# Kernel optimization log

Measured on AMD Instinct MI355X. Metric: run time of the kernel, lower is better.

The kernel has to match this reference:

```python
import jax, jax.numpy as jnp
import numpy as np

C = 1024
H = 16
D = C // H

def setup_inputs() -> dict:
    key = jax.random.key(0)
    ks = jax.random.split(key, 12)
    s = 1.0 / np.sqrt(C)
    inp = {
        "Q": jax.random.normal(ks[0], (2, 1024, C), jnp.float32),
        "K_in": jax.random.normal(ks[1], (2, 4096, C), jnp.float32),
        "V_in": jax.random.normal(ks[2], (2, 4096, C), jnp.float32),
        "V_bias": jax.random.normal(ks[3], (2, 4096), jnp.float32),
        "Wq_w": jax.random.uniform(ks[4], (C, C), jnp.float32, -s, s),
        "Wq_b": jax.random.uniform(ks[5], (C,), jnp.float32, -s, s),
        "Wk_w": jax.random.uniform(ks[6], (C, C), jnp.float32, -s, s),
        "Wk_b": jax.random.uniform(ks[7], (C,), jnp.float32, -s, s),
        "Wv_w": jax.random.uniform(ks[8], (C, C), jnp.float32, -s, s),
        "Wv_b": jax.random.uniform(ks[9], (C,), jnp.float32, -s, s),
        "Wo_w": jax.random.uniform(ks[10], (C, C), jnp.float32, -s, s),
        "Wo_b": jax.random.uniform(ks[11], (C,), jnp.float32, -s, s),
    }
    return inp

def reference(Q, K_in, V_in, V_bias, Wq_w, Wq_b, Wk_w, Wk_b, Wv_w, Wv_b, Wo_w, Wo_b):
    B, Lq, _ = Q.shape
    Lk = K_in.shape[1]
    # linear projections (torch Linear: x @ W.T + b), split heads -> [B,H,L,D]
    q = (Q @ Wq_w.T + Wq_b).reshape(B, Lq, H, D).transpose(0, 2, 1, 3)
    k = (K_in @ Wk_w.T + Wk_b).reshape(B, Lk, H, D).transpose(0, 2, 1, 3)
    v = (V_in @ Wv_w.T + Wv_b).reshape(B, Lk, H, D).transpose(0, 2, 1, 3)
    scale = 1.0 / np.sqrt(D).astype(np.float32)
    logits = jnp.einsum("bhqd,bhkd->bhqk", q, k) * scale
    logits = logits + V_bias[:, None, None, :]  # per-key additive bias
    attn = jax.nn.softmax(logits, axis=-1)      # dropout p=0.0 (eval)
    out = jnp.einsum("bhqk,bhkd->bhqd", attn, v)
    out = out.transpose(0, 2, 1, 3).reshape(B, Lq, C)
    return out @ Wo_w.T + Wo_b
```

## Files before the change

### kernel.cpp

```cpp
#include <hip/hip_runtime.h>


typedef __attribute__((ext_vector_type(8))) __bf16 bf16x8;
typedef __attribute__((ext_vector_type(4))) float f32x4;
typedef __attribute__((ext_vector_type(16))) float f32x16;

#define LOG2E 1.44269504f
#define MFIX 24.0f

__device__ __forceinline__ unsigned short f2bf(float f) {
  union { float f; unsigned u; } v; v.f = f;
  unsigned r = v.u + 0x7fffu + ((v.u >> 16) & 1u);
  return (unsigned short)(r >> 16);
}
__device__ __forceinline__ unsigned short f2h(float x) {
  _Float16 h = (_Float16)x;
  return __builtin_bit_cast(unsigned short, h);
}
__device__ __forceinline__ float h2f(unsigned short u) {
  return (float)__builtin_bit_cast(_Float16, u);
}

__device__ __forceinline__ f32x4 mfma16(bf16x8 a, bf16x8 b, f32x4 c) {
  return __builtin_amdgcn_mfma_f32_16x16x32_bf16(a, b, c, 0, 0, 0);
}
__device__ __forceinline__ f32x16 mfma32(bf16x8 a, bf16x8 b, f32x16 c) {
  return __builtin_amdgcn_mfma_f32_32x32x16_bf16(a, b, c, 0, 0, 0);
}

__device__ __forceinline__ unsigned pk2(float lo, float hi) {
  unsigned short a = __builtin_bit_cast(unsigned short, (__bf16)lo);
  unsigned short b = __builtin_bit_cast(unsigned short, (__bf16)hi);
  return (unsigned)a | ((unsigned)b << 16);
}

template <typename T>
__device__ __forceinline__ void gload16(const T* g, T* l) {
  __builtin_amdgcn_global_load_lds(
      (const __attribute__((address_space(1))) void*)g,
      (__attribute__((address_space(3))) void*)l, 16, 0, 0);
}

struct CvtJob { const float* src; unsigned short* dst; int n4; };
struct CvtArgs { CvtJob j[6]; };

__global__ __launch_bounds__(256) void cvt_kernel(CvtArgs a) {
  const CvtJob jb = a.j[blockIdx.y];
  const float4* s = (const float4*)jb.src;
  unsigned short* d = jb.dst;
  const int stride = gridDim.x * blockDim.x;
  for (int i = blockIdx.x * blockDim.x + threadIdx.x; i < jb.n4; i += stride) {
    float4 f = s[i];
    ushort4 u;
    u.x = f2bf(f.x); u.y = f2bf(f.y); u.z = f2bf(f.z); u.w = f2bf(f.w);
    ((ushort4*)d)[i] = u;
  }
}

__global__ __launch_bounds__(256) void prep_kb(const float* __restrict__ Vb,
                                               unsigned* __restrict__ kb) {
  const int i = blockIdx.x * 256 + threadIdx.x;
  const float x = Vb[i] * LOG2E;
  const unsigned short h = f2bf(x);
  union { unsigned u; float f; } hf; hf.u = (unsigned)h << 16;
  const unsigned short lo = f2bf(x - hf.f);
  kb[i] = (unsigned)h | ((unsigned)lo << 16);
}

struct ProjSeg {
  const unsigned short* A; const unsigned short* W; const float* bias;
  void* out; int mode; int Llog2; float oscale;
};
struct ProjArgs { ProjSeg s[2]; int start1; };

__global__ __launch_bounds__(256, 2) void proj_gemm(ProjArgs pa) {
  constexpr int K = 1024;
  __shared__ unsigned short Alds[2][128][64];
  __shared__ unsigned short Blds[2][128][64];

  const int bid = blockIdx.x;
  const int si = (bid >= pa.start1) ? 1 : 0;
  const ProjSeg sg = pa.s[si];
  const int local = bid - (si ? pa.start1 : 0);
  const int xcd = local & 7, jj = local >> 3;
  const int m0 = ((jj >> 3) * 8 + xcd) * 128;
  const int n0 = (jj & 7) * 128;

  const int tid = threadIdx.x;
  const int wid = tid >> 6, l = tid & 63;
  const int wr = wid >> 1, wc = wid & 1;
  const int lg = l >> 4, lm = l & 15;

  const int srow = wid * 8 + (l >> 3);
  const int scol = ((l & 7) ^ (l >> 3)) * 8;
  const unsigned short* aS = sg.A + (long)(m0 + srow) * K + scol;
  const unsigned short* bS = sg.W + (long)(n0 + srow) * K + scol;

  f32x4 acc[4][4] = {};

  auto issue = [&](int kt, int buf) {
#pragma unroll
    for (int c = 0; c < 4; ++c) {
      gload16(aS + ((long)c * 32) * K + kt * 64,
              &Alds[buf][c * 32 + wid * 8][0]);
      gload16(bS + ((long)c * 32) * K + kt * 64,
              &Blds[buf][c * 32 + wid * 8][0]);
    }
  };

  issue(0, 0);
  issue(1, 1);

  for (int t = 0; t < 16; ++t) {
    if (t < 15) asm volatile("s_waitcnt vmcnt(8)" ::: "memory");
    else        asm volatile("s_waitcnt vmcnt(0)" ::: "memory");
    __builtin_amdgcn_sched_barrier(0);
    __builtin_amdgcn_s_barrier();
    const int buf = t & 1;

#pragma unroll
    for (int kc = 0; kc < 2; ++kc) {
      bf16x8 af[4], bf[4];
#pragma unroll
      for (int i = 0; i < 4; ++i) {
        const int so = ((kc * 4 + lg) ^ (lm & 7)) * 8;
        af[i] = *(const bf16x8*)&Alds[buf][wr * 64 + i * 16 + lm][so];
        bf[i] = *(const bf16x8*)&Blds[buf][wc * 64 + i * 16 + lm][so];
      }
      __builtin_amdgcn_s_setprio(1);
      if (sg.mode == 1) {
#pragma unroll
        for (int i = 0; i < 4; ++i)
#pragma unroll
          for (int j = 0; j < 4; ++j)
            acc[i][j] = mfma16(bf[i], af[j], acc[i][j]);
      } else {
#pragma unroll
        for (int i = 0; i < 4; ++i)
#pragma unroll
          for (int j = 0; j < 4; ++j)
            acc[i][j] = mfma16(af[i], bf[j], acc[i][j]);
      }
      __builtin_amdgcn_s_setprio(0);
    }

    __builtin_amdgcn_s_barrier();
    if (t + 2 < 16) issue(t + 2, buf);
  }

  const int rr = lg * 4;
  if (sg.mode == 0) {
    const int Lmask = (1 << sg.Llog2) - 1;
    unsigned short* out = (unsigned short*)sg.out;
#pragma unroll
    for (int j = 0; j < 4; ++j) {
      const int n = n0 + wc * 64 + j * 16 + lm;
      const float bv = sg.bias[n];
      const int h = n >> 6, d = n & 63;
#pragma unroll
      for (int i = 0; i < 4; ++i)
#pragma unroll
        for (int r = 0; r < 4; ++r) {
          const int m = m0 + wr * 64 + i * 16 + rr + r;
          const int b = m >> sg.Llog2, li = m & Lmask;
          const long o = (((long)(b * 16 + h) << sg.Llog2) + li) * 64 + d;
          out[o] = f2bf((acc[i][j][r] + bv) * sg.oscale);
        }
    }
  } else if (sg.mode == 1) {
    unsigned short* out = (unsigned short*)sg.out;
#pragma unroll
    for (int i = 0; i < 4; ++i)
#pragma unroll
      for (int r = 0; r < 4; ++r) {
        const int n = n0 + wc * 64 + i * 16 + rr + r;
        const float bv = sg.bias[n];
        const int h = n >> 6, d = n & 63;
#pragma unroll
        for (int j = 0; j < 4; ++j) {
          const int m = m0 + wr * 64 + j * 16 + lm;
          const int b = m >> 12, lk = m & 4095;
          const long o = ((long)((b * 16 + h) * 64 + d)) * 4096 + lk;
          out[o] = f2bf(acc[i][j][r] + bv);
        }
      }
  } else {
    float* out = (float*)sg.out;
#pragma unroll
    for (int j = 0; j < 4; ++j) {
      const int n = n0 + wc * 64 + j * 16 + lm;
      const float bv = sg.bias[n];
#pragma unroll
      for (int i = 0; i < 4; ++i)
#pragma unroll
        for (int r = 0; r < 4; ++r) {
          const int m = m0 + wr * 64 + i * 16 + rr + r;
          out[(long)m * 1024 + n] = acc[i][j][r] + bv;
        }
    }
  }
}

__global__ __launch_bounds__(256, 2) void attn64(
    const unsigned short* __restrict__ qh, const unsigned short* __restrict__ kh,
    const unsigned short* __restrict__ vT, const unsigned* __restrict__ kb,
    unsigned short* __restrict__ Oh, float* __restrict__ ml, int nt) {
  __shared__ unsigned short Klds[2][64][64];
  __shared__ unsigned short Vlds[2][64][64];

  const int tid = threadIdx.x;
  const int wid = tid >> 6, lane = tid & 63;
  const int lq = lane & 31, hi = lane >> 5;
  const int bh = blockIdx.x, qb = blockIdx.y, sp = blockIdx.z;
  const int b = bh >> 4;
  const int qA = qb * 256 + wid * 64 + lq;
  const int kt0 = sp * nt;

  bf16x8 qrA[4], qrB[4];
  {
    const unsigned short* qp = qh + ((long)bh * 1024 + qA) * 64 + hi * 8;
#pragma unroll
    for (int dc = 0; dc < 4; ++dc) {
      qrA[dc] = *(const bf16x8*)(qp + dc * 16);
      qrB[dc] = *(const bf16x8*)(qp + 32 * 64 + dc * 16);
    }
  }

  union uv { uint4 u; bf16x8 v; };
  uv bq; bq.u = make_uint4(hi ? 0u : 0x3F803F80u, 0u, 0u, 0u);

  auto swap23 = [](int r) { return (r & 0x33) | ((r & 4) << 1) | ((r & 8) >> 1); };
  const int r0 = wid * 16 + (lane >> 3), r1 = r0 + 8;
  const int s0 = ((lane & 7) ^ (r0 & 7)) * 8;
  const int s1 = ((lane & 7) ^ (r1 & 7)) * 8;
  const unsigned short* kg0 =
      kh + ((long)bh * 4096 + kt0 * 64 + swap23(r0)) * 64 + s0;
  const unsigned short* kg1 =
      kh + ((long)bh * 4096 + kt0 * 64 + swap23(r1)) * 64 + s1;
  const unsigned short* vg0 = vT + ((long)bh * 64 + r0) * 4096 + kt0 * 64 + s0;
  const unsigned short* vg1 = vT + ((long)bh * 64 + r1) * 4096 + kt0 * 64 + s1;
  const unsigned* kbp = kb + b * 4096 + kt0 * 64;
  const int kbkey = swap23(lq);

  unsigned kbw0[2], kbw1[2];
  auto issue = [&](int t, int buf) {
    gload16(kg0 + (long)t * 4096, &Klds[buf][wid * 16][0]);
    gload16(kg1 + (long)t * 4096, &Klds[buf][wid * 16 + 8][0]);
    gload16(vg0 + t * 64, &Vlds[buf][wid * 16][0]);
    gload16(vg1 + t * 64, &Vlds[buf][wid * 16 + 8][0]);
    kbw0[buf] = kbp[t * 64 + kbkey];
    kbw1[buf] = kbp[t * 64 + 32 + kbkey];
  };
  issue(0, 0);
  issue(1, 1);

  const int rsw = lq & 7;
  float lA = 0.f, lB = 0.f;
  f32x16 oaA0 = {}, oaA1 = {}, oaB0 = {}, oaB1 = {};
  uv puA[4], puB[4];

  auto softmax = [&](const f32x16& sx0, const f32x16& sx1, float& lreg,
                     uv* pu) {
    float p[32];
#pragma unroll
    for (int r = 0; r < 16; ++r) {
      p[r] = __builtin_amdgcn_exp2f(sx0[r] - MFIX);
      p[16 + r] = __builtin_amdgcn_exp2f(sx1[r] - MFIX);
    }
    float s16[16];
#pragma unroll
    for (int i = 0; i < 16; ++i) s16[i] = p[i] + p[i + 16];
#pragma unroll
    for (int s = 8; s > 0; s >>= 1)
#pragma unroll
      for (int i = 0; i < 8; ++i)
        if (i < s) s16[i] += s16[i + s];
    lreg += s16[0] + __shfl_xor(s16[0], 32);
#pragma unroll
    for (int kc = 0; kc < 4; ++kc)
      pu[kc].u = make_uint4(pk2(p[kc * 8 + 0], p[kc * 8 + 1]),
                            pk2(p[kc * 8 + 2], p[kc * 8 + 3]),
                            pk2(p[kc * 8 + 4], p[kc * 8 + 5]),
                            pk2(p[kc * 8 + 6], p[kc * 8 + 7]));
  };

  for (int t = 0; t < nt; ++t) {
    const int buf = t & 1;
    if (t < nt - 1) asm volatile("s_waitcnt vmcnt(6)" ::: "memory");
    else            asm volatile("s_waitcnt vmcnt(0)" ::: "memory");
    __builtin_amdgcn_sched_barrier(0);
    __builtin_amdgcn_s_barrier();

    uv ka0, ka1;
    ka0.u = make_uint4(hi ? 0u : kbw0[buf], 0u, 0u, 0u);
    ka1.u = make_uint4(hi ? 0u : kbw1[buf], 0u, 0u, 0u);

    bf16x8 kf0[4], kf1[4];
#pragma unroll
    for (int dc = 0; dc < 4; ++dc) {
      const int so = ((dc * 2 + hi) ^ rsw) * 8;
      kf0[dc] = *(const bf16x8*)&Klds[buf][lq][so];
      kf1[dc] = *(const bf16x8*)&Klds[buf][32 + lq][so];
    }

    f32x16 sa0 = {}, sa1 = {}, sb0 = {}, sb1 = {};
    __builtin_amdgcn_s_setprio(1);
#pragma unroll
    for (int dc = 0; dc < 4; ++dc) {
      sa0 = mfma32(kf0[dc], qrA[dc], sa0);
      sa1 = mfma32(kf1[dc], qrA[dc], sa1);
      sb0 = mfma32(kf0[dc], qrB[dc], sb0);
      sb1 = mfma32(kf1[dc], qrB[dc], sb1);
    }
    sa0 = mfma32(ka0.v, bq.v, sa0);
    sa1 = mfma32(ka1.v, bq.v, sa1);
    sb0 = mfma32(ka0.v, bq.v, sb0);
    sb1 = mfma32(ka1.v, bq.v, sb1);
    __builtin_amdgcn_s_setprio(0);

    softmax(sa0, sa1, lA, puA);

    bf16x8 vf0[4], vf1[4];
#pragma unroll
    for (int kc = 0; kc < 4; ++kc) {
      const int so = ((kc * 2 + hi) ^ rsw) * 8;
      vf0[kc] = *(const bf16x8*)&Vlds[buf][lq][so];
      vf1[kc] = *(const bf16x8*)&Vlds[buf][32 + lq][so];
    }

    __builtin_amdgcn_s_setprio(1);
#pragma unroll
    for (int kc = 0; kc < 4; ++kc) {
      oaA0 = mfma32(vf0[kc], puA[kc].v, oaA0);
      oaA1 = mfma32(vf1[kc], puA[kc].v, oaA1);
    }
    __builtin_amdgcn_s_setprio(0);

    softmax(sb0, sb1, lB, puB);

    __builtin_amdgcn_s_setprio(1);
#pragma unroll
    for (int kc = 0; kc < 4; ++kc) {
      oaB0 = mfma32(vf0[kc], puB[kc].v, oaB0);
      oaB1 = mfma32(vf1[kc], puB[kc].v, oaB1);
    }
    __builtin_amdgcn_s_setprio(0);

    __builtin_amdgcn_s_barrier();
    if (t + 2 < nt) issue(t + 2, buf);
  }

  const float invA = 1.0f / lA, invB = 1.0f / lB;
  unsigned short* obA = Oh + (((long)sp * 32 + bh) * 1024 + qA) * 64 + hi * 4;
  unsigned short* obB = obA + 32 * 64;
#pragma unroll
  for (int g = 0; g < 4; ++g) {
    ushort4 u;
    u.x = f2h(oaA0[g * 4 + 0] * invA); u.y = f2h(oaA0[g * 4 + 1] * invA);
    u.z = f2h(oaA0[g * 4 + 2] * invA); u.w = f2h(oaA0[g * 4 + 3] * invA);
    *(ushort4*)(obA + g * 8) = u;
    u.x = f2h(oaA1[g * 4 + 0] * invA); u.y = f2h(oaA1[g * 4 + 1] * invA);
    u.z = f2h(oaA1[g * 4 + 2] * invA); u.w = f2h(oaA1[g * 4 + 3] * invA);
    *(ushort4*)(obA + 32 + g * 8) = u;
    u.x = f2h(oaB0[g * 4 + 0] * invB); u.y = f2h(oaB0[g * 4 + 1] * invB);
    u.z = f2h(oaB0[g * 4 + 2] * invB); u.w = f2h(oaB0[g * 4 + 3] * invB);
    *(ushort4*)(obB + g * 8) = u;
    u.x = f2h(oaB1[g * 4 + 0] * invB); u.y = f2h(oaB1[g * 4 + 1] * invB);
    u.z = f2h(oaB1[g * 4 + 2] * invB); u.w = f2h(oaB1[g * 4 + 3] * invB);
    *(ushort4*)(obB + 32 + g * 8) = u;
  }
  if (hi == 0) {
    *(float2*)(ml + (((long)sp * 32 + bh) * 1024 + qA) * 2) =
        make_float2(MFIX, lA);
    *(float2*)(ml + (((long)sp * 32 + bh) * 1024 + qA + 32) * 2) =
        make_float2(MFIX, lB);
  }
}

__global__ __launch_bounds__(256) void combineN(
    const unsigned short* __restrict__ Oh, const float* __restrict__ ml,
    unsigned short* __restrict__ ao, int NS) {
  const int idx = blockIdx.x * 256 + threadIdx.x;
  const int bh = idx >> 10, q = idx & 1023;
  const int b = bh >> 4, h = bh & 15;
  float w[8], wsum = 0.f;
  for (int i = 0; i < NS; ++i) {
    w[i] = ml[((long)i * 32768 + idx) * 2 + 1];
    wsum += w[i];
  }
  const float inv = 1.0f / wsum;
  for (int i = 0; i < NS; ++i) w[i] *= inv;

  unsigned short* op = ao + ((long)b * 1024 + q) * 1024 + h * 64;
#pragma unroll
  for (int blk = 0; blk < 8; ++blk) {
    float acc[8] = {};
    for (int i = 0; i < NS; ++i) {
      uint4 u = *(const uint4*)(Oh + ((long)i * 32768 + idx) * 64 + blk * 8);
      const unsigned short* hs = (const unsigned short*)&u;
#pragma unroll
      for (int j = 0; j < 8; ++j) acc[j] += w[i] * h2f(hs[j]);
    }
    ushort4 o0, o1;
    o0.x = f2bf(acc[0]); o0.y = f2bf(acc[1]);
    o0.z = f2bf(acc[2]); o0.w = f2bf(acc[3]);
    o1.x = f2bf(acc[4]); o1.y = f2bf(acc[5]);
    o1.z = f2bf(acc[6]); o1.w = f2bf(acc[7]);
    *(ushort4*)(op + blk * 8) = o0;
    *(ushort4*)(op + blk * 8 + 4) = o1;
  }
}

extern "C" void kernel_launch(void* const* d_in, const int* in_sizes, int n_in,
                              void* d_out, int out_size, void* d_ws,
                              size_t ws_size, hipStream_t stream) {
  const float* Q = (const float*)d_in[0];
  const float* K_in = (const float*)d_in[1];
  const float* V_in = (const float*)d_in[2];
  const float* V_bias = (const float*)d_in[3];
  const float* Wq_w = (const float*)d_in[4];
  const float* Wk_w = (const float*)d_in[6];
  const float* Wv_w = (const float*)d_in[8];
  const float* Wo_w = (const float*)d_in[10];
  const float* Wq_b = (const float*)d_in[5];
  const float* Wk_b = (const float*)d_in[7];
  const float* Wv_b = (const float*)d_in[9];
  const float* Wo_b = (const float*)d_in[11];

  const int NS = (ws_size >= ((81ull << 20))) ? 8 : 4;
  const int nt = 64 / NS;

  char* ws = (char*)d_ws;
  unsigned short* Wqb = (unsigned short*)(ws + (0l << 20));
  float* mlp = (float*)(ws + (0l << 20));
  unsigned short* Wkb = (unsigned short*)(ws + (2l << 20));
  unsigned short* Wvb = (unsigned short*)(ws + (4l << 20));
  unsigned short* Wob = (unsigned short*)(ws + (6l << 20));
  unsigned short* qhp = (unsigned short*)(ws + (8l << 20));
  unsigned short* khp = (unsigned short*)(ws + (12l << 20));
  unsigned short* vTp = (unsigned short*)(ws + (28l << 20));
  unsigned short* Qbf = (unsigned short*)(ws + (44l << 20));
  unsigned short* Kbf = (unsigned short*)(ws + (48l << 20));
  unsigned short* Vbf = (unsigned short*)(ws + (48l << 20));
  unsigned short* Ohp = (unsigned short*)(ws + (44l << 20));
  unsigned short* aop = (unsigned short*)(ws + ((44l + 4 * NS) << 20));
  unsigned* kbp = (unsigned*)(ws + ((48l + 4 * NS) << 20));

  CvtArgs c1;
  c1.j[0] = CvtJob{Wq_w, Wqb, 262144};
  c1.j[1] = CvtJob{Wk_w, Wkb, 262144};
  c1.j[2] = CvtJob{Wv_w, Wvb, 262144};
  c1.j[3] = CvtJob{Wo_w, Wob, 262144};
  c1.j[4] = CvtJob{Q, Qbf, 524288};
  c1.j[5] = CvtJob{K_in, Kbf, 2097152};
  cvt_kernel<<<dim3(512, 6), 256, 0, stream>>>(c1);
  prep_kb<<<32, 256, 0, stream>>>(V_bias, kbp);

  ProjArgs pA;
  pA.s[0] = ProjSeg{Kbf, Wkb, Wk_b, khp, 0, 12, 1.0f};
  pA.s[1] = ProjSeg{Qbf, Wqb, Wq_b, qhp, 0, 10, 0.125f * LOG2E};
  pA.start1 = 512;
  proj_gemm<<<640, 256, 0, stream>>>(pA);

  CvtArgs c2;
  c2.j[0] = CvtJob{V_in, Vbf, 2097152};
  c2.j[1] = c2.j[0]; c2.j[2] = c2.j[0];
  c2.j[3] = c2.j[0]; c2.j[4] = c2.j[0]; c2.j[5] = c2.j[0];
  cvt_kernel<<<dim3(512, 1), 256, 0, stream>>>(c2);

  ProjArgs pB;
  pB.s[0] = ProjSeg{Vbf, Wvb, Wv_b, vTp, 1, 12, 1.0f};
  pB.s[1] = pB.s[0];
  pB.start1 = 1 << 30;
  proj_gemm<<<512, 256, 0, stream>>>(pB);

  attn64<<<dim3(32, 4, NS), 256, 0, stream>>>(qhp, khp, vTp, kbp, Ohp, mlp, nt);
  combineN<<<128, 256, 0, stream>>>(Ohp, mlp, aop, NS);

  ProjArgs pO;
  pO.s[0] = ProjSeg{aop, Wob, Wo_b, d_out, 2, 0, 1.0f};
  pO.s[1] = pO.s[0];
  pO.start1 = 1 << 30;
  proj_gemm<<<128, 256, 0, stream>>>(pO);
}
```

Measured before the change: 211.4 us.

## Triple-buffer attention K/V tiles, stage key bias in LDS, merge V conversion

The attention kernel moves from double to triple buffering of the K/V LDS tiles, so loads run two tiles ahead. The wait counts are adjusted to match. The per-key bias now comes into LDS with one async load instead of per-tile global loads into registers. On the host, split-K is fixed at 4 splits, and when the workspace is large the V_in conversion joins the first conversion launch, removing one kernel launch. The larger LDS footprint may lower occupancy, and fewer splits reduce attention parallelism compared with the previous 8-split path.

```diff
diff --git a/kernel.cpp b/kernel.cpp
--- a/kernel.cpp
+++ b/kernel.cpp
@@ -42,7 +42,7 @@
 }
 
 struct CvtJob { const float* src; unsigned short* dst; int n4; };
-struct CvtArgs { CvtJob j[6]; };
+struct CvtArgs { CvtJob j[7]; };
 
 __global__ __launch_bounds__(256) void cvt_kernel(CvtArgs a) {
   const CvtJob jb = a.j[blockIdx.y];
@@ -205,8 +205,9 @@
     const unsigned short* __restrict__ qh, const unsigned short* __restrict__ kh,
     const unsigned short* __restrict__ vT, const unsigned* __restrict__ kb,
     unsigned short* __restrict__ Oh, float* __restrict__ ml, int nt) {
-  __shared__ unsigned short Klds[2][64][64];
-  __shared__ unsigned short Vlds[2][64][64];
+  __shared__ unsigned short Klds[3][64][64];
+  __shared__ unsigned short Vlds[3][64][64];
+  __shared__ unsigned kblds[1024];
 
   const int tid = threadIdx.x;
   const int wid = tid >> 6, lane = tid & 63;
@@ -239,20 +240,19 @@
       kh + ((long)bh * 4096 + kt0 * 64 + swap23(r1)) * 64 + s1;
   const unsigned short* vg0 = vT + ((long)bh * 64 + r0) * 4096 + kt0 * 64 + s0;
   const unsigned short* vg1 = vT + ((long)bh * 64 + r1) * 4096 + kt0 * 64 + s1;
-  const unsigned* kbp = kb + b * 4096 + kt0 * 64;
   const int kbkey = swap23(lq);
 
-  unsigned kbw0[2], kbw1[2];
-  auto issue = [&](int t, int buf) {
-    gload16(kg0 + (long)t * 4096, &Klds[buf][wid * 16][0]);
-    gload16(kg1 + (long)t * 4096, &Klds[buf][wid * 16 + 8][0]);
-    gload16(vg0 + t * 64, &Vlds[buf][wid * 16][0]);
-    gload16(vg1 + t * 64, &Vlds[buf][wid * 16 + 8][0]);
-    kbw0[buf] = kbp[t * 64 + kbkey];
-    kbw1[buf] = kbp[t * 64 + 32 + kbkey];
+  auto issue = [&](int t, int bufi) {
+    gload16(kg0 + (long)t * 4096, &Klds[bufi][wid * 16][0]);
+    gload16(kg1 + (long)t * 4096, &Klds[bufi][wid * 16 + 8][0]);
+    gload16(vg0 + t * 64, &Vlds[bufi][wid * 16][0]);
+    gload16(vg1 + t * 64, &Vlds[bufi][wid * 16 + 8][0]);
   };
+
+  gload16(kb + b * 4096 + kt0 * 64 + wid * 256 + lane * 4, &kblds[wid * 256]);
   issue(0, 0);
   issue(1, 1);
+  issue(2, 2);
 
   const int rsw = lq & 7;
   float lA = 0.f, lB = 0.f;
@@ -284,16 +284,20 @@
                             pk2(p[kc * 8 + 6], p[kc * 8 + 7]));
   };
 
+  int buf = 0;
   for (int t = 0; t < nt; ++t) {
-    const int buf = t & 1;
-    if (t < nt - 1) asm volatile("s_waitcnt vmcnt(6)" ::: "memory");
-    else            asm volatile("s_waitcnt vmcnt(0)" ::: "memory");
+    if (t < nt - 2)      asm volatile("s_waitcnt vmcnt(8)" ::: "memory");
+    else if (t < nt - 1) asm volatile("s_waitcnt vmcnt(4)" ::: "memory");
+    else                 asm volatile("s_waitcnt vmcnt(0)" ::: "memory");
     __builtin_amdgcn_sched_barrier(0);
     __builtin_amdgcn_s_barrier();
-
+    __builtin_amdgcn_sched_barrier(0);
+
+    const unsigned w0 = kblds[t * 64 + kbkey];
+    const unsigned w1 = kblds[t * 64 + 32 + kbkey];
     uv ka0, ka1;
-    ka0.u = make_uint4(hi ? 0u : kbw0[buf], 0u, 0u, 0u);
-    ka1.u = make_uint4(hi ? 0u : kbw1[buf], 0u, 0u, 0u);
+    ka0.u = make_uint4(hi ? 0u : w0, 0u, 0u, 0u);
+    ka1.u = make_uint4(hi ? 0u : w1, 0u, 0u, 0u);
 
     bf16x8 kf0[4], kf1[4];
 #pragma unroll
@@ -347,7 +351,8 @@
     __builtin_amdgcn_s_setprio(0);
 
     __builtin_amdgcn_s_barrier();
-    if (t + 2 < nt) issue(t + 2, buf);
+    if (t + 3 < nt) issue(t + 3, buf);
+    buf = (buf == 2) ? 0 : buf + 1;
   }
 
   const float invA = 1.0f / lA, invB = 1.0f / lB;
@@ -419,16 +424,16 @@
   const float* V_in = (const float*)d_in[2];
   const float* V_bias = (const float*)d_in[3];
   const float* Wq_w = (const float*)d_in[4];
+  const float* Wq_b = (const float*)d_in[5];
   const float* Wk_w = (const float*)d_in[6];
+  const float* Wk_b = (const float*)d_in[7];
   const float* Wv_w = (const float*)d_in[8];
+  const float* Wv_b = (const float*)d_in[9];
   const float* Wo_w = (const float*)d_in[10];
-  const float* Wq_b = (const float*)d_in[5];
-  const float* Wk_b = (const float*)d_in[7];
-  const float* Wv_b = (const float*)d_in[9];
   const float* Wo_b = (const float*)d_in[11];
 
-  const int NS = (ws_size >= ((81ull << 20))) ? 8 : 4;
-  const int nt = 64 / NS;
+  const int NS = 4, nt = 16;
+  const bool bigws = ws_size >= (81ull << 20);
 
   char* ws = (char*)d_ws;
   unsigned short* Wqb = (unsigned short*)(ws + (0l << 20));
@@ -441,10 +446,10 @@
   unsigned short* vTp = (unsigned short*)(ws + (28l << 20));
   unsigned short* Qbf = (unsigned short*)(ws + (44l << 20));
   unsigned short* Kbf = (unsigned short*)(ws + (48l << 20));
-  unsigned short* Vbf = (unsigned short*)(ws + (48l << 20));
   unsigned short* Ohp = (unsigned short*)(ws + (44l << 20));
-  unsigned short* aop = (unsigned short*)(ws + ((44l + 4 * NS) << 20));
-  unsigned* kbp = (unsigned*)(ws + ((48l + 4 * NS) << 20));
+  unsigned short* aop = (unsigned short*)(ws + (60l << 20));
+  unsigned* kbp = (unsigned*)(ws + (64l << 20));
+  unsigned short* Vbf = bigws ? (unsigned short*)(ws + (65l << 20)) : Kbf;
 
   CvtArgs c1;
   c1.j[0] = CvtJob{Wq_w, Wqb, 262144};
@@ -453,7 +458,8 @@
   c1.j[3] = CvtJob{Wo_w, Wob, 262144};
   c1.j[4] = CvtJob{Q, Qbf, 524288};
   c1.j[5] = CvtJob{K_in, Kbf, 2097152};
-  cvt_kernel<<<dim3(512, 6), 256, 0, stream>>>(c1);
+  c1.j[6] = CvtJob{V_in, Vbf, 2097152};
+  cvt_kernel<<<dim3(512, bigws ? 7 : 6), 256, 0, stream>>>(c1);
   prep_kb<<<32, 256, 0, stream>>>(V_bias, kbp);
 
   ProjArgs pA;
@@ -462,11 +468,12 @@
   pA.start1 = 512;
   proj_gemm<<<640, 256, 0, stream>>>(pA);
 
-  CvtArgs c2;
-  c2.j[0] = CvtJob{V_in, Vbf, 2097152};
-  c2.j[1] = c2.j[0]; c2.j[2] = c2.j[0];
-  c2.j[3] = c2.j[0]; c2.j[4] = c2.j[0]; c2.j[5] = c2.j[0];
-  cvt_kernel<<<dim3(512, 1), 256, 0, stream>>>(c2);
+  if (!bigws) {
+    CvtArgs c2;
+    c2.j[0] = CvtJob{V_in, Vbf, 2097152};
+    for (int i = 1; i < 7; ++i) c2.j[i] = c2.j[0];
+    cvt_kernel<<<dim3(512, 1), 256, 0, stream>>>(c2);
+  }
 
   ProjArgs pB;
   pB.s[0] = ProjSeg{Vbf, Wvb, Wv_b, vTp, 1, 12, 1.0f};
```

New measurement: 171.9 us. 18.6% less time.
